# Performance work log

Measured on AMD Instinct MI355X. Metric: run time of the kernel, lower is better.

The kernel has to match this reference:

```python
import jax, jax.numpy as jnp
import numpy as np

N_NODES = 100000
N_EDGES = 1_600_000
D = 64
E_POS = 20000
NEG = 100


def setup_inputs() -> dict:
    key = jax.random.key(0)
    ks = jax.random.split(key, 10)
    s = 1.0 / np.sqrt(D)
    return {
        "features": jax.random.normal(ks[0], (N_NODES, D), dtype=jnp.float32),
        "W1": jax.random.normal(ks[1], (D, D), dtype=jnp.float32) * s,
        "b1": jnp.zeros((D,), dtype=jnp.float32),
        "W2": jax.random.normal(ks[2], (D, D), dtype=jnp.float32) * s,
        "b2": jnp.zeros((D,), dtype=jnp.float32),
        "src": jax.random.randint(ks[3], (N_EDGES,), 0, N_NODES, dtype=jnp.int32),
        "dst": jax.random.randint(ks[4], (N_EDGES,), 0, N_NODES, dtype=jnp.int32),
        "pos_src": jax.random.randint(ks[5], (E_POS,), 0, N_NODES, dtype=jnp.int32),
        "pos_dst": jax.random.randint(ks[6], (E_POS,), 0, N_NODES, dtype=jnp.int32),
        "neg_src": jax.random.randint(ks[7], (E_POS * NEG,), 0, N_NODES, dtype=jnp.int32),
        "neg_dst": jax.random.randint(ks[8], (E_POS * NEG,), 0, N_NODES, dtype=jnp.int32),
        "neg_sample_size": NEG,
    }


def _sage_gcn(h, src, dst, W, b, n):
    # DGL SAGEConv 'gcn' aggregator: (sum of in-neighbor feats + self) / (in_deg + 1), then Linear
    neigh = jax.ops.segment_sum(h[src], dst, num_segments=n)           # [N, D]
    deg = jax.ops.segment_sum(jnp.ones((src.shape[0],), h.dtype), dst, num_segments=n)
    h_neigh = (neigh + h) / (deg[:, None] + 1.0)
    return h_neigh @ W + b


def reference(features, W1, b1, W2, b2, src, dst, pos_src, pos_dst, neg_src, neg_dst, neg_sample_size):
    n = features.shape[0]
    h = jax.nn.relu(_sage_gcn(features, src, dst, W1, b1, n))
    emb = _sage_gcn(h, src, dst, W2, b2, n)                            # [N, D]
    pos_score = jnp.sum(emb[pos_src] * emb[pos_dst], axis=1)           # [E_pos]
    neg_score = jnp.sum(emb[neg_src] * emb[neg_dst], axis=1)           # [E_pos*NEG]
    pos_ls = jax.nn.log_sigmoid(pos_score)
    neg_ls = jax.nn.log_sigmoid(-neg_score).reshape(-1, neg_sample_size)
    return jnp.mean(-pos_ls - jnp.sum(neg_ls, axis=1))
```

## Files before the change

### kernel.cpp

```cpp
#include <hip/hip_runtime.h>
#include <hip/hip_fp16.h>
#include <math.h>

#define D 64
#define NPB 64
#define NPB_SHIFT 6
#define LCAP 2560
#define NPART 512
#define NV 2

typedef _Float16 half4v __attribute__((ext_vector_type(4)));
typedef float f32x4 __attribute__((ext_vector_type(4)));
typedef float f32x2v __attribute__((ext_vector_type(2)));


__global__ void scan1_kernel(const int* __restrict__ in, int* __restrict__ out,
                             int* __restrict__ bsum, int n) {
    __shared__ int s[1024];
    int t = threadIdx.x;
    int i = blockIdx.x * 1024 + t;
    int v = (i < n) ? in[i] : 0;
    s[t] = v;
    __syncthreads();
    for (int off = 1; off < 1024; off <<= 1) {
        int add = (t >= off) ? s[t - off] : 0;
        __syncthreads();
        s[t] += add;
        __syncthreads();
    }
    if (i < n) out[i] = s[t] - v;
    if (t == 1023) bsum[blockIdx.x] = s[1023];
}

__global__ void scan2_kernel(int* __restrict__ bsum, int nb) {
    __shared__ int s[1024];
    int t = threadIdx.x;
    int v = (t < nb) ? bsum[t] : 0;
    s[t] = v;
    __syncthreads();
    for (int off = 1; off < 1024; off <<= 1) {
        int add = (t >= off) ? s[t - off] : 0;
        __syncthreads();
        s[t] += add;
        __syncthreads();
    }
    if (t < nb) bsum[t] = s[t] - v;
}


__global__ __launch_bounds__(256) void hist_f2f8_kernel(
    const int* __restrict__ dst, int* __restrict__ harr,
    int e, int nb, int chunk,
    const float* __restrict__ fin, unsigned char* __restrict__ f8out, int n4)
{
    extern __shared__ int sh[];
    if ((int)blockIdx.x < NPART) {
        const int p = blockIdx.x;
        for (int i = threadIdx.x; i < nb; i += 256) sh[i] = 0;
        __syncthreads();
        const int s = p * chunk, ee = min(e, s + chunk);
        for (int i = s + threadIdx.x; i < ee; i += 256)
            atomicAdd(&sh[dst[i] >> NPB_SHIFT], 1);
        __syncthreads();
        for (int b = threadIdx.x; b < nb; b += 256) harr[b * NPART + p] = sh[b];
    } else {
        int i = (blockIdx.x - NPART) * 256 + threadIdx.x;
        if (i < n4) {
            float4 v = *(const float4*)(fin + (size_t)i * 4);
            int pk0 = __builtin_amdgcn_cvt_pk_fp8_f32(v.x, v.y, 0, false);
            int pk1 = __builtin_amdgcn_cvt_pk_fp8_f32(v.z, v.w, 0, false);
            ((unsigned int*)f8out)[i] = (unsigned int)(pk0 & 0xFFFF) | ((unsigned int)(pk1 & 0xFFFF) << 16);
        }
    }
}

__global__ __launch_bounds__(256) void part_scatter_kernel(
    const int* __restrict__ src, const int* __restrict__ dst,
    const int* __restrict__ soff, const int* __restrict__ bsum,
    int* __restrict__ packed, int e, int nb, int chunk)
{
    extern __shared__ int cur[];
    const int p = blockIdx.x;
    for (int b = threadIdx.x; b < nb; b += 256) {
        int idx = b * NPART + p;
        cur[b] = soff[idx] + bsum[idx >> 10];
    }
    __syncthreads();
    const int s = p * chunk, ee = min(e, s + chunk);
    for (int i = s + threadIdx.x; i < ee; i += 256) {
        int d = dst[i];
        int pos = atomicAdd(&cur[d >> NPB_SHIFT], 1);
        packed[pos] = src[i] | ((d & (NPB - 1)) << 24);
    }
}

__global__ __launch_bounds__(256) void bucket_build_kernel(
    const int* __restrict__ soff, const int* __restrict__ bsum,
    const int* __restrict__ packed,
    int* __restrict__ csr, int* __restrict__ rs,
    int n, int e_total, int nb)
{
    __shared__ int lcsr[LCAP];
    __shared__ int dcount[NPB];
    __shared__ int dexcl[NPB];
    __shared__ int cur2[NPB];
    const int b    = blockIdx.x;
    const int i0x  = b * NPART;
    const int base = soff[i0x] + bsum[i0x >> 10];
    int end;
    if (b + 1 < nb) {
        const int i1x = (b + 1) * NPART;
        end = soff[i1x] + bsum[i1x >> 10];
    } else {
        end = e_total;
    }
    const int cnt  = end - base;
    const int nb0  = b << NPB_SHIFT;
    const int nnode = min(NPB, n - nb0);
    const int tid  = threadIdx.x;

    if (tid < NPB) { dcount[tid] = 0; cur2[tid] = 0; }
    __syncthreads();

    for (int i = tid; i < cnt; i += 256)
        atomicAdd(&dcount[(packed[base + i] >> 24) & (NPB - 1)], 1);
    __syncthreads();
    if (tid == 0) {
        int run = 0;
        for (int t = 0; t < nnode; ++t) { dexcl[t] = run; run += dcount[t]; }
    }
    __syncthreads();
    if (tid < nnode) rs[nb0 + tid] = base + dexcl[tid];

    if (cnt <= LCAP) {
        for (int i = tid; i < cnt; i += 256) {
            int pk = packed[base + i];
            int ln = (pk >> 24) & (NPB - 1);
            int pos = dexcl[ln] + atomicAdd(&cur2[ln], 1);
            lcsr[pos] = pk & 0xFFFFFF;
        }
        __syncthreads();
        for (int i = tid; i < cnt; i += 256) csr[base + i] = lcsr[i];
    } else {
        for (int i = tid; i < cnt; i += 256) {
            int pk = packed[base + i];
            int ln = (pk >> 24) & (NPB - 1);
            int pos = dexcl[ln] + atomicAdd(&cur2[ln], 1);
            csr[base + pos] = pk & 0xFFFFFF;
        }
    }
}


__device__ __forceinline__ void cvt8(int2 w, float* x) {
    f32x2v a0 = __builtin_amdgcn_cvt_pk_f32_fp8(w.x, false);
    f32x2v a1 = __builtin_amdgcn_cvt_pk_f32_fp8(w.x, true);
    f32x2v a2 = __builtin_amdgcn_cvt_pk_f32_fp8(w.y, false);
    f32x2v a3 = __builtin_amdgcn_cvt_pk_f32_fp8(w.y, true);
    x[0] = a0[0]; x[1] = a0[1]; x[2] = a1[0]; x[3] = a1[1];
    x[4] = a2[0]; x[5] = a2[1]; x[6] = a3[0]; x[7] = a3[1];
}


__global__ __launch_bounds__(256) void agg_kernel(
    const unsigned char* __restrict__ in8, const int* __restrict__ csr,
    const int* __restrict__ rs, __half* __restrict__ anorm,
    int n, int e_total)
{
    const int ll = threadIdx.x & 7;
    const int g  = (blockIdx.x * 256 + threadIdx.x) >> 3;
    const int v0 = g * NV;
    if (v0 >= n) return;

    #pragma unroll
    for (int t = 0; t < NV; ++t) {
        const int v = v0 + t;
        if (v >= n) break;
        const int i0 = rs[v];
        const int i1 = (v + 1 < n) ? rs[v + 1] : e_total;
        const int m  = i1 - i0;

        float acc[8];
        #pragma unroll
        for (int j = 0; j < 8; ++j) acc[j] = 0.0f;

        int2 f0, f1, f2, f3;
        if (m > 0) f0 = *(const int2*)(in8 + ((size_t)csr[i0] << 6) + (ll << 3));
        if (m > 1) f1 = *(const int2*)(in8 + ((size_t)csr[i0 + 1] << 6) + (ll << 3));
        if (m > 2) f2 = *(const int2*)(in8 + ((size_t)csr[i0 + 2] << 6) + (ll << 3));
        if (m > 3) f3 = *(const int2*)(in8 + ((size_t)csr[i0 + 3] << 6) + (ll << 3));
        for (int i = 0; i < m; ++i) {
            int2 fn;
            if (i + 4 < m) fn = *(const int2*)(in8 + ((size_t)csr[i0 + i + 4] << 6) + (ll << 3));
            float x[8]; cvt8(f0, x);
            #pragma unroll
            for (int j = 0; j < 8; ++j) acc[j] += x[j];
            f0 = f1; f1 = f2; f2 = f3; f3 = fn;
        }

        int2 sf = *(const int2*)(in8 + ((size_t)v << 6) + (ll << 3));
        float sx[8]; cvt8(sf, sx);
        const float inv = 1.0f / (float)(m + 1);
        union { __half h[8]; float4 f; } u;
        #pragma unroll
        for (int j = 0; j < 8; ++j) u.h[j] = __float2half((acc[j] + sx[j]) * inv);
        *(float4*)(anorm + (size_t)v * D + ll * 8) = u.f;
    }
}


template<int RELU>
__global__ __launch_bounds__(256) void post_mfma_kernel(
    const __half* __restrict__ anorm, unsigned char* __restrict__ out8,
    const float* __restrict__ W, const float* __restrict__ bias, int n)
{
    const int lane = threadIdx.x & 63;
    const int w    = threadIdx.x >> 6;
    const int tile = blockIdx.x * 4 + w;
    const int v0   = tile * 16;
    if (v0 >= n) return;

    const int col = lane & 15;
    const int kb  = (lane >> 4) * 4;

    half4v bf[4][4];
    #pragma unroll
    for (int kt = 0; kt < 4; ++kt)
        #pragma unroll
        for (int t = 0; t < 4; ++t)
            #pragma unroll
            for (int j = 0; j < 4; ++j)
                bf[kt][t][j] = (_Float16)W[(kt * 16 + kb + j) * D + t * 16 + col];

    int vr = v0 + col; if (vr >= n) vr = n - 1;
    const __half* ap = anorm + (size_t)vr * D + kb;
    half4v af[4];
    #pragma unroll
    for (int kt = 0; kt < 4; ++kt)
        af[kt] = *(const half4v*)(ap + kt * 16);

    f32x4 c[4];
    #pragma unroll
    for (int t = 0; t < 4; ++t) {
        float bv = bias[t * 16 + col];
        c[t] = (f32x4){bv, bv, bv, bv};
    }
    #pragma unroll
    for (int kt = 0; kt < 4; ++kt)
        #pragma unroll
        for (int t = 0; t < 4; ++t)
            c[t] = __builtin_amdgcn_mfma_f32_16x16x16f16(af[kt], bf[kt][t], c[t], 0, 0, 0);

    #pragma unroll
    for (int t = 0; t < 4; ++t)
        #pragma unroll
        for (int p = 0; p < 4; ++p) {
            int r = v0 + (lane >> 4) * 4 + p;
            if (r < n) {
                float o = c[t][p];
                if (RELU) o = fmaxf(o, 0.0f);
                int pk = __builtin_amdgcn_cvt_pk_fp8_f32(o, o, 0, false);
                out8[(size_t)r * D + t * 16 + col] = (unsigned char)(pk & 0xFF);
            }
        }
}


__device__ __forceinline__ float softplus_fast(float x) {
    return fmaxf(x, 0.0f) + __logf(1.0f + __expf(-fabsf(x)));
}

__global__ __launch_bounds__(256) void score_both_kernel(
    const unsigned char* __restrict__ emb8,
    const int* __restrict__ pos_src, const int* __restrict__ pos_dst,
    const int* __restrict__ neg_src, const int* __restrict__ neg_dst,
    int ep, int eneg, int pblocks, double* __restrict__ accum)
{
    const int* a_idx; const int* b_idx;
    int npairs, bid, nblk;
    float sign;
    if ((int)blockIdx.x < pblocks) {
        a_idx = pos_src; b_idx = pos_dst; npairs = ep; sign = -1.0f;
        bid = blockIdx.x; nblk = pblocks;
    } else {
        a_idx = neg_src; b_idx = neg_dst; npairs = eneg; sign = 1.0f;
        bid = blockIdx.x - pblocks; nblk = gridDim.x - pblocks;
    }

    const int lane = threadIdx.x & 63;
    const int gw   = (bid * 256 + (int)threadIdx.x) >> 6;
    const int nw   = (nblk * 256) >> 6;
    const int ntiles = (npairs + 15) >> 4;
    const int ftiles = npairs >> 4;

    const int pr = lane & 15;
    const int ks = lane >> 4;
    const bool has = (ks == (pr >> 2));
    const int reg  = pr & 3;

    float local = 0.0f;

    int t = gw;
    for (; t + 3 * nw < ftiles; t += 4 * nw) {
        int ti[4] = {t, t + nw, t + 2 * nw, t + 3 * nw};
        long av[4][2], bv[4][2];
        #pragma unroll
        for (int u = 0; u < 4; ++u) {
            int p0 = ti[u] * 16 + pr;
            int ia = a_idx[p0], ib = b_idx[p0];
            const unsigned char* pa = emb8 + ((size_t)ia << 6) + ks * 8;
            const unsigned char* pb = emb8 + ((size_t)ib << 6) + ks * 8;
            av[u][0] = *(const long*)pa;
            av[u][1] = *(const long*)(pa + 32);
            bv[u][0] = *(const long*)pb;
            bv[u][1] = *(const long*)(pb + 32);
        }
        #pragma unroll
        for (int u = 0; u < 4; ++u) {
            f32x4 cv = {0.f, 0.f, 0.f, 0.f};
            cv = __builtin_amdgcn_mfma_f32_16x16x32_fp8_fp8(av[u][0], bv[u][0], cv, 0, 0, 0);
            cv = __builtin_amdgcn_mfma_f32_16x16x32_fp8_fp8(av[u][1], bv[u][1], cv, 0, 0, 0);
            if (has) local += softplus_fast(sign * cv[reg]);
        }
    }
    for (; t < ntiles; t += nw) {
        int p0 = t * 16 + pr;
        int c0 = min(p0, npairs - 1);
        int ia = a_idx[c0], ib = b_idx[c0];
        const unsigned char* pa = emb8 + ((size_t)ia << 6) + ks * 8;
        const unsigned char* pb = emb8 + ((size_t)ib << 6) + ks * 8;
        long a0 = *(const long*)pa;
        long a1 = *(const long*)(pa + 32);
        long b0 = *(const long*)pb;
        long b1 = *(const long*)(pb + 32);
        f32x4 cv = {0.f, 0.f, 0.f, 0.f};
        cv = __builtin_amdgcn_mfma_f32_16x16x32_fp8_fp8(a0, b0, cv, 0, 0, 0);
        cv = __builtin_amdgcn_mfma_f32_16x16x32_fp8_fp8(a1, b1, cv, 0, 0, 0);
        if (has && p0 < npairs) local += softplus_fast(sign * cv[reg]);
    }

    __shared__ float red[256];
    red[threadIdx.x] = local;
    __syncthreads();
    for (int s = blockDim.x / 2; s > 0; s >>= 1) {
        if ((int)threadIdx.x < s) red[threadIdx.x] += red[threadIdx.x + s];
        __syncthreads();
    }
    if (threadIdx.x == 0) atomicAdd(accum, (double)red[0]);
}

__global__ void finalize_kernel(const double* __restrict__ acc, float* __restrict__ out, int ep) {
    if (threadIdx.x == 0 && blockIdx.x == 0)
        out[0] = (float)(acc[0] / (double)ep);
}


extern "C" void kernel_launch(void* const* d_in, const int* in_sizes, int n_in,
                              void* d_out, int out_size, void* d_ws, size_t ws_size,
                              hipStream_t stream) {
    const float* features = (const float*)d_in[0];
    const float* W1 = (const float*)d_in[1];
    const float* b1 = (const float*)d_in[2];
    const float* W2 = (const float*)d_in[3];
    const float* b2 = (const float*)d_in[4];
    const int* src     = (const int*)d_in[5];
    const int* dst     = (const int*)d_in[6];
    const int* pos_src = (const int*)d_in[7];
    const int* pos_dst = (const int*)d_in[8];
    const int* neg_src = (const int*)d_in[9];
    const int* neg_dst = (const int*)d_in[10];

    const int N    = in_sizes[0] / D;
    const int E    = in_sizes[5];
    const int EP   = in_sizes[7];
    const int ENEG = in_sizes[9];
    const int NB   = (N + NPB - 1) >> NPB_SHIFT;

    char* ws = (char*)d_ws;
    size_t off = 0;
    auto alloc = [&](size_t bytes) -> void* {
        void* p = ws + off;
        off += (bytes + 255) & ~(size_t)255;
        return p;
    };
    int*    rs     = (int*)alloc((size_t)(N + 64) * 4);
    int*    harr   = (int*)alloc((size_t)NB * NPART * 4);
    int*    soff   = (int*)alloc((size_t)NB * NPART * 4);
    int*    bsum   = (int*)alloc(1024 * 4);
    int*    packed = (int*)alloc((size_t)E * 4);
    int*    csr    = (int*)alloc((size_t)E * 4);
    __half* anorm  = (__half*)alloc((size_t)N * D * 2);
    unsigned char* feat8 = (unsigned char*)alloc((size_t)N * D);
    unsigned char* h8    = (unsigned char*)alloc((size_t)N * D);
    unsigned char* emb8  = (unsigned char*)alloc((size_t)N * D);
    double* acc    = (double*)alloc(8);

    hipMemsetAsync(acc, 0, 8, stream);

    const int chunk = (E + NPART - 1) / NPART;
    const size_t ldsNB = (size_t)NB * 4;
    const int n4 = (N * D) / 4;

    hist_f2f8_kernel<<<NPART + (n4 + 255) / 256, 256, ldsNB, stream>>>(
        dst, harr, E, NB, chunk, features, feat8, n4);
    const int scn = NB * NPART;
    const int nbs = (scn + 1023) / 1024;
    scan1_kernel<<<nbs, 1024, 0, stream>>>(harr, soff, bsum, scn);
    scan2_kernel<<<1, 1024, 0, stream>>>(bsum, nbs);
    part_scatter_kernel<<<NPART, 256, ldsNB, stream>>>(src, dst, soff, bsum, packed, E, NB, chunk);
    bucket_build_kernel<<<NB, 256, 0, stream>>>(soff, bsum, packed, csr, rs, N, E, NB);

    const int ngroups = (N + NV - 1) / NV;
    const int ab = (ngroups * 8 + 255) / 256;
    const int ntiles16 = (N + 15) / 16;
    const int pb2 = (ntiles16 + 3) / 4;

    agg_kernel<<<ab, 256, 0, stream>>>(feat8, csr, rs, anorm, N, E);
    post_mfma_kernel<1><<<pb2, 256, 0, stream>>>(anorm, h8, W1, b1, N);

    agg_kernel<<<ab, 256, 0, stream>>>(h8, csr, rs, anorm, N, E);
    post_mfma_kernel<0><<<pb2, 256, 0, stream>>>(anorm, emb8, W2, b2, N);

    int pbp = ((EP + 15) / 16 + 3) / 4;  if (pbp > 2048) pbp = 2048; if (pbp < 1) pbp = 1;
    int pbn = ((ENEG + 15) / 16 + 3) / 4; if (pbn > 2048) pbn = 2048;
    score_both_kernel<<<pbp + pbn, 256, 0, stream>>>(
        emb8, pos_src, pos_dst, neg_src, neg_dst, EP, ENEG, pbp, acc);

    finalize_kernel<<<1, 64, 0, stream>>>(acc, (float*)d_out, EP);
}
```

Baseline: 217.4 us.

## Quantize embeddings to FP4 with global amax scale for scoring gathers

Adds a global abs-max reduction in the second linear layer and a new kernel that requantizes the fp8 embeddings to 4-bit E2M1 codes with a per-tensor scale. The scoring kernel then gathers half as many bytes per node and expands the nibbles back to fp8 with byte-permute before the fp8 MFMA, rescaling the dot product. The goal is to cut the random-gather memory traffic of the 2M negative-pair scoring. The cost is an extra kernel pass over the embeddings, an atomic max, and a large loss of numerical precision in the scores.

```diff
diff --git a/kernel.cpp b/kernel.cpp
--- a/kernel.cpp
+++ b/kernel.cpp
@@ -209,10 +209,11 @@
 }
 
 
-template<int RELU>
+template<int RELU, int AMAX>
 __global__ __launch_bounds__(256) void post_mfma_kernel(
     const __half* __restrict__ anorm, unsigned char* __restrict__ out8,
-    const float* __restrict__ W, const float* __restrict__ bias, int n)
+    const float* __restrict__ W, const float* __restrict__ bias, int n,
+    unsigned int* __restrict__ amax)
 {
     const int lane = threadIdx.x & 63;
     const int w    = threadIdx.x >> 6;
@@ -251,6 +252,7 @@
         for (int t = 0; t < 4; ++t)
             c[t] = __builtin_amdgcn_mfma_f32_16x16x16f16(af[kt], bf[kt][t], c[t], 0, 0, 0);
 
+    float lm = 0.0f;
     #pragma unroll
     for (int t = 0; t < 4; ++t)
         #pragma unroll
@@ -259,10 +261,56 @@
             if (r < n) {
                 float o = c[t][p];
                 if (RELU) o = fmaxf(o, 0.0f);
+                if (AMAX) lm = fmaxf(lm, fabsf(o));
                 int pk = __builtin_amdgcn_cvt_pk_fp8_f32(o, o, 0, false);
                 out8[(size_t)r * D + t * 16 + col] = (unsigned char)(pk & 0xFF);
             }
         }
+    if (AMAX) {
+        #pragma unroll
+        for (int s = 1; s < 64; s <<= 1) lm = fmaxf(lm, __shfl_xor(lm, s));
+        if (lane == 0) atomicMax(amax, __float_as_uint(lm));
+    }
+}
+
+
+__global__ __launch_bounds__(256) void quant4_kernel(
+    const unsigned char* __restrict__ emb8, unsigned int* __restrict__ emb4,
+    const unsigned int* __restrict__ amax, int ngroups)
+{
+    int gid = blockIdx.x * 256 + threadIdx.x;
+    if (gid >= ngroups) return;
+    float am = __uint_as_float(*amax);
+    float scale = 6.0f / fmaxf(am, 1e-20f);
+    int2 w = *(const int2*)(emb8 + (size_t)gid * 8);
+    float x[8]; cvt8(w, x);
+    unsigned out = 0;
+    #pragma unroll
+    for (int j = 0; j < 4; ++j) {
+        #pragma unroll
+        for (int h = 0; h < 2; ++h) {
+            float v = x[j + h * 4] * scale;
+            float a = fabsf(v);
+            unsigned t = (unsigned)(a > 0.25f) + (a > 0.75f) + (a > 1.25f) + (a > 1.75f)
+                       + (a > 2.5f) + (a > 3.5f) + (a > 5.0f);
+            unsigned nib = t | (v < 0.0f ? 8u : 0u);
+            out |= nib << (j * 8 + h * 4);
+        }
+    }
+    emb4[gid] = out;
+}
+
+
+__device__ __forceinline__ long fp4_to_fp8x8(unsigned w) {
+    const unsigned POOL_LO = 0x3C383000u;
+    const unsigned POOL_HI = 0x4C484440u;
+    unsigned sel_lo = w & 0x07070707u;
+    unsigned sel_hi = (w >> 4) & 0x07070707u;
+    unsigned sg_lo  = (w & 0x08080808u) << 4;
+    unsigned sg_hi  = ((w >> 4) & 0x08080808u) << 4;
+    unsigned lo = __builtin_amdgcn_perm(POOL_HI, POOL_LO, sel_lo) | sg_lo;
+    unsigned hi = __builtin_amdgcn_perm(POOL_HI, POOL_LO, sel_hi) | sg_hi;
+    return (long)(((unsigned long)hi << 32) | (unsigned long)lo);
 }
 
 
@@ -271,10 +319,11 @@
 }
 
 __global__ __launch_bounds__(256) void score_both_kernel(
-    const unsigned char* __restrict__ emb8,
+    const unsigned int* __restrict__ emb4,
     const int* __restrict__ pos_src, const int* __restrict__ pos_dst,
     const int* __restrict__ neg_src, const int* __restrict__ neg_dst,
-    int ep, int eneg, int pblocks, double* __restrict__ accum)
+    int ep, int eneg, int pblocks, const unsigned int* __restrict__ amax,
+    double* __restrict__ accum)
 {
     const int* a_idx; const int* b_idx;
     int npairs, bid, nblk;
@@ -287,6 +336,9 @@
         bid = blockIdx.x - pblocks; nblk = gridDim.x - pblocks;
     }
 
+    float am = __uint_as_float(*amax);
+    const float invS2 = (am * am) / 36.0f;
+
     const int lane = threadIdx.x & 63;
     const int gw   = (bid * 256 + (int)threadIdx.x) >> 6;
     const int nw   = (nblk * 256) >> 6;
@@ -303,40 +355,36 @@
     int t = gw;
     for (; t + 3 * nw < ftiles; t += 4 * nw) {
         int ti[4] = {t, t + nw, t + 2 * nw, t + 3 * nw};
-        long av[4][2], bv[4][2];
+        unsigned wa0[4], wa1[4], wb0[4], wb1[4];
         #pragma unroll
         for (int u = 0; u < 4; ++u) {
             int p0 = ti[u] * 16 + pr;
-            int ia = a_idx[p0], ib = b_idx[p0];
-            const unsigned char* pa = emb8 + ((size_t)ia << 6) + ks * 8;
-            const unsigned char* pb = emb8 + ((size_t)ib << 6) + ks * 8;
-            av[u][0] = *(const long*)pa;
-            av[u][1] = *(const long*)(pa + 32);
-            bv[u][0] = *(const long*)pb;
-            bv[u][1] = *(const long*)(pb + 32);
+            size_t ba = (size_t)a_idx[p0] * 8;
+            size_t bb = (size_t)b_idx[p0] * 8;
+            wa0[u] = emb4[ba + ks];
+            wa1[u] = emb4[ba + ks + 4];
+            wb0[u] = emb4[bb + ks];
+            wb1[u] = emb4[bb + ks + 4];
         }
         #pragma unroll
         for (int u = 0; u < 4; ++u) {
             f32x4 cv = {0.f, 0.f, 0.f, 0.f};
-            cv = __builtin_amdgcn_mfma_f32_16x16x32_fp8_fp8(av[u][0], bv[u][0], cv, 0, 0, 0);
-            cv = __builtin_amdgcn_mfma_f32_16x16x32_fp8_fp8(av[u][1], bv[u][1], cv, 0, 0, 0);
-            if (has) local += softplus_fast(sign * cv[reg]);
+            cv = __builtin_amdgcn_mfma_f32_16x16x32_fp8_fp8(fp4_to_fp8x8(wa0[u]), fp4_to_fp8x8(wb0[u]), cv, 0, 0, 0);
+            cv = __builtin_amdgcn_mfma_f32_16x16x32_fp8_fp8(fp4_to_fp8x8(wa1[u]), fp4_to_fp8x8(wb1[u]), cv, 0, 0, 0);
+            if (has) local += softplus_fast(sign * cv[reg] * invS2);
         }
     }
     for (; t < ntiles; t += nw) {
         int p0 = t * 16 + pr;
         int c0 = min(p0, npairs - 1);
-        int ia = a_idx[c0], ib = b_idx[c0];
-        const unsigned char* pa = emb8 + ((size_t)ia << 6) + ks * 8;
-        const unsigned char* pb = emb8 + ((size_t)ib << 6) + ks * 8;
-        long a0 = *(const long*)pa;
-        long a1 = *(const long*)(pa + 32);
-        long b0 = *(const long*)pb;
-        long b1 = *(const long*)(pb + 32);
+        size_t ba = (size_t)a_idx[c0] * 8;
+        size_t bb = (size_t)b_idx[c0] * 8;
+        unsigned a0 = emb4[ba + ks], a1 = emb4[ba + ks + 4];
+        unsigned b0 = emb4[bb + ks], b1 = emb4[bb + ks + 4];
         f32x4 cv = {0.f, 0.f, 0.f, 0.f};
-        cv = __builtin_amdgcn_mfma_f32_16x16x32_fp8_fp8(a0, b0, cv, 0, 0, 0);
-        cv = __builtin_amdgcn_mfma_f32_16x16x32_fp8_fp8(a1, b1, cv, 0, 0, 0);
-        if (has && p0 < npairs) local += softplus_fast(sign * cv[reg]);
+        cv = __builtin_amdgcn_mfma_f32_16x16x32_fp8_fp8(fp4_to_fp8x8(a0), fp4_to_fp8x8(b0), cv, 0, 0, 0);
+        cv = __builtin_amdgcn_mfma_f32_16x16x32_fp8_fp8(fp4_to_fp8x8(a1), fp4_to_fp8x8(b1), cv, 0, 0, 0);
+        if (has && p0 < npairs) local += softplus_fast(sign * cv[reg] * invS2);
     }
 
     __shared__ float red[256];
@@ -393,9 +441,12 @@
     unsigned char* feat8 = (unsigned char*)alloc((size_t)N * D);
     unsigned char* h8    = (unsigned char*)alloc((size_t)N * D);
     unsigned char* emb8  = (unsigned char*)alloc((size_t)N * D);
+    unsigned int*  emb4  = (unsigned int*)alloc((size_t)N * D / 2);
+    unsigned int*  amax  = (unsigned int*)alloc(4);
     double* acc    = (double*)alloc(8);
 
     hipMemsetAsync(acc, 0, 8, stream);
+    hipMemsetAsync(amax, 0, 4, stream);
 
     const int chunk = (E + NPART - 1) / NPART;
     const size_t ldsNB = (size_t)NB * 4;
@@ -416,15 +467,18 @@
     const int pb2 = (ntiles16 + 3) / 4;
 
     agg_kernel<<<ab, 256, 0, stream>>>(feat8, csr, rs, anorm, N, E);
-    post_mfma_kernel<1><<<pb2, 256, 0, stream>>>(anorm, h8, W1, b1, N);
+    post_mfma_kernel<1, 0><<<pb2, 256, 0, stream>>>(anorm, h8, W1, b1, N, nullptr);
 
     agg_kernel<<<ab, 256, 0, stream>>>(h8, csr, rs, anorm, N, E);
-    post_mfma_kernel<0><<<pb2, 256, 0, stream>>>(anorm, emb8, W2, b2, N);
+    post_mfma_kernel<0, 1><<<pb2, 256, 0, stream>>>(anorm, emb8, W2, b2, N, amax);
+
+    const int ng8 = N * D / 8;
+    quant4_kernel<<<(ng8 + 255) / 256, 256, 0, stream>>>(emb8, emb4, amax, ng8);
 
     int pbp = ((EP + 15) / 16 + 3) / 4;  if (pbp > 2048) pbp = 2048; if (pbp < 1) pbp = 1;
     int pbn = ((ENEG + 15) / 16 + 3) / 4; if (pbn > 2048) pbn = 2048;
     score_both_kernel<<<pbp + pbn, 256, 0, stream>>>(
-        emb8, pos_src, pos_dst, neg_src, neg_dst, EP, ENEG, pbp, acc);
+        emb4, pos_src, pos_dst, neg_src, neg_dst, EP, ENEG, pbp, amax, acc);
 
     finalize_kernel<<<1, 64, 0, stream>>>(acc, (float*)d_out, EP);
 }
```

Measured after the change: 289.4 us. 1.33x slower.
